# Kernel optimization log

Hardware: AMD Instinct MI355X
Metric: run time of the kernel (lower is better)

The kernel has to match this reference:

```python
import jax, jax.numpy as jnp
import numpy as np

M, K, N = 8192, 4096, 4096


def setup_inputs() -> dict:
    key = jax.random.key(0)
    k1, k2, k3 = jax.random.split(key, 3)
    inp = jax.random.normal(k1, (M, K), dtype=jnp.float32)
    weight = jax.random.normal(k2, (N, K), dtype=jnp.float32)
    bias = jax.random.normal(k3, (N,), dtype=jnp.bfloat16)
    return {"inp": inp, "weight": weight, "bias": bias}


def reference(inp, weight, bias):
    # FP8TensorMeta scales are all ones in the source module.
    scale = jnp.float32(1.0)       # quantization scale
    scale_inv = jnp.float32(1.0)   # dequantization scale (per operand)

    # cast_to_fp8: scale then saturate-cast to e4m3
    inp_fp8 = (inp * scale).astype(jnp.float8_e4m3fn)
    weight_fp8 = (weight * scale).astype(jnp.float8_e4m3fn)

    # fp8_gemm: dequantized GEMM with fp32 accumulation, bf16 bias, fp32 out
    out = jnp.einsum(
        "mk,nk->mn",
        inp_fp8.astype(jnp.float32),
        weight_fp8.astype(jnp.float32),
    ) * (scale_inv * scale_inv)
    out = out + bias.astype(jnp.float32)[None, :]
    return out
```

## Files before the change

### kernel.cpp

```cpp
#include <hip/hip_runtime.h>
#include <hip/hip_bf16.h>
#include <stdint.h>


#define MD 8192
#define KD 4096
#define ND 4096
#define BM 256
#define BN 128
#define BK 64

using f32x16 = __attribute__((ext_vector_type(16))) float;
using i32x4  = __attribute__((ext_vector_type(4))) int;
using i32x8  = __attribute__((ext_vector_type(8))) int;

__device__ __forceinline__ int q4(float4 f) {
  int v = 0;
  v = __builtin_amdgcn_cvt_pk_fp8_f32(f.x, f.y, v, false);
  v = __builtin_amdgcn_cvt_pk_fp8_f32(f.z, f.w, v, true);
  return v;
}

__global__ __launch_bounds__(256) void quant_fp8_fused_kernel(
    const float* __restrict__ inA, const float* __restrict__ inW,
    uint8_t* __restrict__ outA, uint8_t* __restrict__ outW) {
  const int NA16 = MD * KD / 16;
  const int NW16 = ND * KD / 16;
  const int tid = blockIdx.x * blockDim.x + threadIdx.x;
  const int stride = gridDim.x * blockDim.x;

  for (int i = tid; i < NA16; i += stride) {
    const float4* p = (const float4*)inA + (size_t)i * 4;
    int4 v = make_int4(q4(p[0]), q4(p[1]), q4(p[2]), q4(p[3]));
    ((int4*)outA)[i] = v;
  }
  for (int i = tid; i < NW16; i += stride) {
    const float4* p = (const float4*)inW + (size_t)i * 4;
    int4 v = make_int4(q4(p[0]), q4(p[1]), q4(p[2]), q4(p[3]));
    ((int4*)outW)[i] = v;
  }
}

__device__ __forceinline__ void gload16(const uint8_t* g, uint8_t* l) {
  __builtin_amdgcn_global_load_lds(
      (const __attribute__((address_space(1))) void*)g,
      (__attribute__((address_space(3))) void*)l, 16, 0, 0);
}

__global__ __launch_bounds__(256, 2) void fp8mx_gemm_bias_kernel(
    const uint8_t* __restrict__ A, const uint8_t* __restrict__ B,
    const __hip_bfloat16* __restrict__ bias, float* __restrict__ C) {
  __shared__ uint8_t sm[3][24576];

  const int bid = blockIdx.x;
  const int xcd = bid & 7;
  const int local = bid >> 3;
  const int grp = local >> 3, li = local & 7;
  const int tm = xcd * 4 + (grp >> 3) * 2 + (li >> 2);
  const int tn = (grp & 7) * 4 + (li & 3);

  const int t = threadIdx.x;
  const int w = t >> 6;
  const int l = t & 63;
  const int wm = w >> 1, wn = w & 1;
  const int r31 = l & 31, kh = l >> 5;

  const int row_s = t >> 2;
  const int gsw = (t & 3) ^ ((row_s >> 1) & 3);
  const size_t abase = (size_t)(tm * BM + row_s) * KD + gsw * 16;
  const size_t bbase = (size_t)(tn * BN + row_s) * KD + gsw * 16;
  const int wd = w * 1024;

  const int s = (r31 >> 1) & 3;
  const int cLo = (((kh << 1) | 0) ^ s) * 16;
  const int cHi = (((kh << 1) | 1) ^ s) * 16;

  f32x16 acc[4][2];
#pragma unroll
  for (int fm = 0; fm < 4; ++fm)
#pragma unroll
    for (int fn = 0; fn < 2; ++fn)
#pragma unroll
      for (int r = 0; r < 16; ++r) acc[fm][fn][r] = 0.f;

  auto stage = [&](int buf, int kt) {
    const size_t ko = (size_t)kt * BK;
    uint8_t* la = &sm[buf][wd];
#pragma unroll
    for (int rnd = 0; rnd < 4; ++rnd)
      gload16(A + abase + (size_t)rnd * 64 * KD + ko, la + rnd * 4096);
    uint8_t* lb = &sm[buf][16384 + wd];
#pragma unroll
    for (int rnd = 0; rnd < 2; ++rnd)
      gload16(B + bbase + (size_t)rnd * 64 * KD + ko, lb + rnd * 4096);
  };

  auto compute = [&](int buf) {
    const uint8_t* sa = &sm[buf][0];
    const uint8_t* sb = &sm[buf][16384];
    i32x8 af[4], bf[2];
#pragma unroll
    for (int fm = 0; fm < 4; ++fm) {
      const int ra = (wm * 128 + fm * 32 + r31) * 64;
      i32x4 lo = *(const i32x4*)(sa + ra + cLo);
      i32x4 hi = *(const i32x4*)(sa + ra + cHi);
#pragma unroll
      for (int j = 0; j < 4; ++j) { af[fm][j] = lo[j]; af[fm][4 + j] = hi[j]; }
    }
#pragma unroll
    for (int fn = 0; fn < 2; ++fn) {
      const int rb = (wn * 64 + fn * 32 + r31) * 64;
      i32x4 lo = *(const i32x4*)(sb + rb + cLo);
      i32x4 hi = *(const i32x4*)(sb + rb + cHi);
#pragma unroll
      for (int j = 0; j < 4; ++j) { bf[fn][j] = lo[j]; bf[fn][4 + j] = hi[j]; }
    }
#pragma unroll
    for (int fm = 0; fm < 4; ++fm)
#pragma unroll
      for (int fn = 0; fn < 2; ++fn)
        acc[fm][fn] = __builtin_amdgcn_mfma_scale_f32_32x32x64_f8f6f4(
            af[fm], bf[fn], acc[fm][fn],
            0, 0,
            0, 0x7F7F7F7F,
            0, 0x7F7F7F7F);
  };

  const int NT = KD / BK;
  stage(0, 0);
  stage(1, 1);
#pragma unroll 1
  for (int kt = 0; kt < NT - 1; ++kt) {
    asm volatile("s_waitcnt vmcnt(6)" ::: "memory");
    __builtin_amdgcn_s_barrier();
    if (kt + 2 < NT) stage((kt + 2) % 3, kt + 2);
    compute(kt % 3);
  }
  asm volatile("s_waitcnt vmcnt(0)" ::: "memory");
  __builtin_amdgcn_s_barrier();
  compute((NT - 1) % 3);

#pragma unroll
  for (int fn = 0; fn < 2; ++fn) {
    const int col = tn * BN + wn * 64 + fn * 32 + r31;
    const float bv = __bfloat162float(bias[col]);
#pragma unroll
    for (int fm = 0; fm < 4; ++fm) {
      const int row0 = tm * BM + wm * 128 + fm * 32 + 4 * kh;
      const f32x16 v = acc[fm][fn];
#pragma unroll
      for (int r = 0; r < 16; ++r) {
        const int row = row0 + (r & 3) + 8 * (r >> 2);
        C[(size_t)row * ND + col] = v[r] + bv;
      }
    }
  }
}

extern "C" void kernel_launch(void* const* d_in, const int* in_sizes, int n_in,
                              void* d_out, int out_size, void* d_ws, size_t ws_size,
                              hipStream_t stream) {
  const float* inp = (const float*)d_in[0];
  const float* wgt = (const float*)d_in[1];
  const __hip_bfloat16* bias = (const __hip_bfloat16*)d_in[2];
  float* out = (float*)d_out;

  uint8_t* a8 = (uint8_t*)d_ws;
  uint8_t* b8 = a8 + (size_t)MD * KD;

  quant_fp8_fused_kernel<<<2048, 256, 0, stream>>>(inp, wgt, a8, b8);
  fp8mx_gemm_bias_kernel<<<1024, 256, 0, stream>>>(a8, b8, bias, out);
}
```

Measured before the change: 395.2 us.

## Enlarge GEMM tile to 256x256 with 512 threads and double-buffered LDS

The GEMM block tile grows from 256x128 to 256x256 and runs with 512 threads (8 waves in a 2x4 layout), so each block reuses its A tile across twice as many output columns and global/L2 traffic per output drops. The LDS pipeline moves from three stages to two, with two barriers per k-step, and the tile-to-block mapping is simplified. The compute loop interleaves LDS fragment loads with MFMA groups wrapped in s_setprio to favour matrix issue. The trade-off is less prefetch depth and more barrier synchronisation, plus possible occupancy limits from the larger block and LDS use.

```diff
diff --git a/kernel.cpp b/kernel.cpp
--- a/kernel.cpp
+++ b/kernel.cpp
@@ -7,7 +7,7 @@
 #define KD 4096
 #define ND 4096
 #define BM 256
-#define BN 128
+#define BN 256
 #define BK 64
 
 using f32x16 = __attribute__((ext_vector_type(16))) float;
@@ -47,22 +47,21 @@
       (__attribute__((address_space(3))) void*)l, 16, 0, 0);
 }
 
-__global__ __launch_bounds__(256, 2) void fp8mx_gemm_bias_kernel(
+__global__ __launch_bounds__(512, 2) void fp8mx_gemm_bias_kernel(
     const uint8_t* __restrict__ A, const uint8_t* __restrict__ B,
     const __hip_bfloat16* __restrict__ bias, float* __restrict__ C) {
-  __shared__ uint8_t sm[3][24576];
+  __shared__ uint8_t sm[2][32768];
 
   const int bid = blockIdx.x;
   const int xcd = bid & 7;
-  const int local = bid >> 3;
-  const int grp = local >> 3, li = local & 7;
-  const int tm = xcd * 4 + (grp >> 3) * 2 + (li >> 2);
-  const int tn = (grp & 7) * 4 + (li & 3);
+  const int li = bid >> 3;
+  const int tm = xcd * 4 + (li >> 4);
+  const int tn = li & 15;
 
   const int t = threadIdx.x;
   const int w = t >> 6;
   const int l = t & 63;
-  const int wm = w >> 1, wn = w & 1;
+  const int wm = w >> 2, wn = w & 3;
   const int r31 = l & 31, kh = l >> 5;
 
   const int row_s = t >> 2;
@@ -85,60 +84,78 @@
 
   auto stage = [&](int buf, int kt) {
     const size_t ko = (size_t)kt * BK;
-    uint8_t* la = &sm[buf][wd];
+    gload16(A + abase + ko, &sm[buf][wd]);
+    gload16(A + abase + (size_t)128 * KD + ko, &sm[buf][8192 + wd]);
+    gload16(B + bbase + ko, &sm[buf][16384 + wd]);
+    gload16(B + bbase + (size_t)128 * KD + ko, &sm[buf][24576 + wd]);
+  };
+
+  auto ldA = [&](const uint8_t* sa, int fm) -> i32x8 {
+    const int ra = (wm * 128 + fm * 32 + r31) * 64;
+    i32x4 lo = *(const i32x4*)(sa + ra + cLo);
+    i32x4 hi = *(const i32x4*)(sa + ra + cHi);
+    i32x8 f;
 #pragma unroll
-    for (int rnd = 0; rnd < 4; ++rnd)
-      gload16(A + abase + (size_t)rnd * 64 * KD + ko, la + rnd * 4096);
-    uint8_t* lb = &sm[buf][16384 + wd];
+    for (int j = 0; j < 4; ++j) { f[j] = lo[j]; f[4 + j] = hi[j]; }
+    return f;
+  };
+  auto ldB = [&](const uint8_t* sb, int fn) -> i32x8 {
+    const int rb = (wn * 64 + fn * 32 + r31) * 64;
+    i32x4 lo = *(const i32x4*)(sb + rb + cLo);
+    i32x4 hi = *(const i32x4*)(sb + rb + cHi);
+    i32x8 f;
 #pragma unroll
-    for (int rnd = 0; rnd < 2; ++rnd)
-      gload16(B + bbase + (size_t)rnd * 64 * KD + ko, lb + rnd * 4096);
+    for (int j = 0; j < 4; ++j) { f[j] = lo[j]; f[4 + j] = hi[j]; }
+    return f;
   };
 
   auto compute = [&](int buf) {
     const uint8_t* sa = &sm[buf][0];
     const uint8_t* sb = &sm[buf][16384];
-    i32x8 af[4], bf[2];
-#pragma unroll
-    for (int fm = 0; fm < 4; ++fm) {
-      const int ra = (wm * 128 + fm * 32 + r31) * 64;
-      i32x4 lo = *(const i32x4*)(sa + ra + cLo);
-      i32x4 hi = *(const i32x4*)(sa + ra + cHi);
-#pragma unroll
-      for (int j = 0; j < 4; ++j) { af[fm][j] = lo[j]; af[fm][4 + j] = hi[j]; }
-    }
-#pragma unroll
-    for (int fn = 0; fn < 2; ++fn) {
-      const int rb = (wn * 64 + fn * 32 + r31) * 64;
-      i32x4 lo = *(const i32x4*)(sb + rb + cLo);
-      i32x4 hi = *(const i32x4*)(sb + rb + cHi);
-#pragma unroll
-      for (int j = 0; j < 4; ++j) { bf[fn][j] = lo[j]; bf[fn][4 + j] = hi[j]; }
-    }
-#pragma unroll
-    for (int fm = 0; fm < 4; ++fm)
-#pragma unroll
-      for (int fn = 0; fn < 2; ++fn)
-        acc[fm][fn] = __builtin_amdgcn_mfma_scale_f32_32x32x64_f8f6f4(
-            af[fm], bf[fn], acc[fm][fn],
-            0, 0,
-            0, 0x7F7F7F7F,
-            0, 0x7F7F7F7F);
+    i32x8 bf0 = ldB(sb, 0), bf1 = ldB(sb, 1);
+    i32x8 af0 = ldA(sa, 0), af1 = ldA(sa, 1);
+    __builtin_amdgcn_s_setprio(1);
+    acc[0][0] = __builtin_amdgcn_mfma_scale_f32_32x32x64_f8f6f4(
+        af0, bf0, acc[0][0], 0, 0, 0, 0x7F7F7F7F, 0, 0x7F7F7F7F);
+    acc[0][1] = __builtin_amdgcn_mfma_scale_f32_32x32x64_f8f6f4(
+        af0, bf1, acc[0][1], 0, 0, 0, 0x7F7F7F7F, 0, 0x7F7F7F7F);
+    acc[1][0] = __builtin_amdgcn_mfma_scale_f32_32x32x64_f8f6f4(
+        af1, bf0, acc[1][0], 0, 0, 0, 0x7F7F7F7F, 0, 0x7F7F7F7F);
+    acc[1][1] = __builtin_amdgcn_mfma_scale_f32_32x32x64_f8f6f4(
+        af1, bf1, acc[1][1], 0, 0, 0, 0x7F7F7F7F, 0, 0x7F7F7F7F);
+    __builtin_amdgcn_s_setprio(0);
+    i32x8 af2 = ldA(sa, 2), af3 = ldA(sa, 3);
+    __builtin_amdgcn_s_setprio(1);
+    acc[2][0] = __builtin_amdgcn_mfma_scale_f32_32x32x64_f8f6f4(
+        af2, bf0, acc[2][0], 0, 0, 0, 0x7F7F7F7F, 0, 0x7F7F7F7F);
+    acc[2][1] = __builtin_amdgcn_mfma_scale_f32_32x32x64_f8f6f4(
+        af2, bf1, acc[2][1], 0, 0, 0, 0x7F7F7F7F, 0, 0x7F7F7F7F);
+    acc[3][0] = __builtin_amdgcn_mfma_scale_f32_32x32x64_f8f6f4(
+        af3, bf0, acc[3][0], 0, 0, 0, 0x7F7F7F7F, 0, 0x7F7F7F7F);
+    acc[3][1] = __builtin_amdgcn_mfma_scale_f32_32x32x64_f8f6f4(
+        af3, bf1, acc[3][1], 0, 0, 0, 0x7F7F7F7F, 0, 0x7F7F7F7F);
+    __builtin_amdgcn_s_setprio(0);
   };
 
   const int NT = KD / BK;
   stage(0, 0);
   stage(1, 1);
+  asm volatile("s_waitcnt vmcnt(4)" ::: "memory");
+  __builtin_amdgcn_s_barrier();
 #pragma unroll 1
-  for (int kt = 0; kt < NT - 1; ++kt) {
-    asm volatile("s_waitcnt vmcnt(6)" ::: "memory");
+  for (int kt = 0; kt < NT; ++kt) {
+    const int c = kt & 1;
+    compute(c);
+    if (kt == NT - 1) break;
     __builtin_amdgcn_s_barrier();
-    if (kt + 2 < NT) stage((kt + 2) % 3, kt + 2);
-    compute(kt % 3);
+    if (kt + 2 < NT) {
+      stage(c, kt + 2);
+      asm volatile("s_waitcnt vmcnt(4)" ::: "memory");
+    } else {
+      asm volatile("s_waitcnt vmcnt(0)" ::: "memory");
+    }
+    __builtin_amdgcn_s_barrier();
   }
-  asm volatile("s_waitcnt vmcnt(0)" ::: "memory");
-  __builtin_amdgcn_s_barrier();
-  compute((NT - 1) % 3);
 
 #pragma unroll
   for (int fn = 0; fn < 2; ++fn) {
@@ -169,5 +186,5 @@
   uint8_t* b8 = a8 + (size_t)MD * KD;
 
   quant_fp8_fused_kernel<<<2048, 256, 0, stream>>>(inp, wgt, a8, b8);
-  fp8mx_gemm_bias_kernel<<<1024, 256, 0, stream>>>(a8, b8, bias, out);
+  fp8mx_gemm_bias_kernel<<<512, 512, 0, stream>>>(a8, b8, bias, out);
 }
```

Result: no change. 399.5 us (+1.1%).
